# Kernel tuning notes

Measured on AMD Instinct MI355X. Metric: run time of the kernel, lower is better.

## Reference

```python
import jax, jax.numpy as jnp
import numpy as np

N = 50000      # nodes
E = 800000     # edges (avg degree 16)
F = 80         # hidden_channels (forced by Linear(80, 1))
L = 4          # num_layers
NG = 1024      # graphs in batch
NFEAT = 9      # OGB atom feature columns
VOCAB = 119    # max atom feature vocab
EPS_BN = 1e-5
EPS_STD = 1e-5


def setup_inputs() -> dict:
    key = jax.random.key(0)
    ks = jax.random.split(key, 20)
    s = 0.05
    x = jax.random.randint(ks[0], (N, NFEAT), 0, 2)
    edge_index = jax.random.randint(ks[1], (2, E), 0, N)
    batch = jnp.sort(jax.random.randint(ks[2], (N,), 0, NG))
    # avg_deg['log'] from the degree histogram == mean over nodes of log(deg+1)
    deg = jax.ops.segment_sum(jnp.ones((E,), jnp.float32), edge_index[1], num_segments=N)
    avg_deg_log = jnp.array([jnp.mean(jnp.log(deg + 1.0))], jnp.float32)
    atom_emb = jax.random.normal(ks[3], (NFEAT, VOCAB, F), jnp.float32) * s
    pre_W = jax.random.normal(ks[4], (L, 2 * F, F), jnp.float32) * s
    pre_b = jax.random.normal(ks[5], (L, F), jnp.float32) * s
    post_W = jax.random.normal(ks[6], (L, 13 * F, F), jnp.float32) * s
    post_b = jax.random.normal(ks[7], (L, F), jnp.float32) * s
    lin_W = jax.random.normal(ks[8], (L, F, F), jnp.float32) * s
    lin_b = jax.random.normal(ks[9], (L, F), jnp.float32) * s
    bn_gamma = 1.0 + jax.random.normal(ks[10], (L, F), jnp.float32) * 0.1
    bn_beta = jax.random.normal(ks[11], (L, F), jnp.float32) * 0.1
    bn_mean = jax.random.normal(ks[12], (L, F), jnp.float32) * 0.1
    bn_var = 0.5 + jax.random.uniform(ks[13], (L, F), jnp.float32)
    mlp_W = jax.random.normal(ks[14], (F, 1), jnp.float32) * s
    mlp_b = jax.random.normal(ks[15], (1,), jnp.float32) * s
    return {
        'x': x, 'edge_index': edge_index, 'batch': batch,
        'avg_deg_log': avg_deg_log, 'atom_emb': atom_emb,
        'pre_W': pre_W, 'pre_b': pre_b, 'post_W': post_W, 'post_b': post_b,
        'lin_W': lin_W, 'lin_b': lin_b,
        'bn_gamma': bn_gamma, 'bn_beta': bn_beta, 'bn_mean': bn_mean, 'bn_var': bn_var,
        'mlp_W': mlp_W, 'mlp_b': mlp_b,
    }


def _forward(x, edge_index, batch, avg_deg_log, atom_emb, pre_W, pre_b,
             post_W, post_b, lin_W, lin_b, bn_gamma, bn_beta, bn_mean, bn_var,
             mlp_W, mlp_b):
    # AtomEncoder: sum of per-column embeddings
    h = jnp.sum(atom_emb[jnp.arange(NFEAT)[None, :], x], axis=1)  # [N, F]
    src, dst = edge_index[0], edge_index[1]
    deg = jax.ops.segment_sum(jnp.ones((E,), h.dtype), dst, num_segments=N)
    has_edge = (deg > 0)[:, None]
    degc = jnp.maximum(deg, 1.0)[:, None]          # clamp(min=1)
    logd = jnp.log(degc + 1.0)                     # [N, 1]
    avg = avg_deg_log[0]
    for i in range(L):
        x_h = h
        # message: pre_nn(cat([x_i, x_j]))
        m = jnp.concatenate([h[dst], h[src]], axis=-1) @ pre_W[i] + pre_b[i]  # [E, F]
        s1 = jax.ops.segment_sum(m, dst, num_segments=N)
        s2 = jax.ops.segment_sum(m * m, dst, num_segments=N)
        mean = s1 / degc
        var = s2 / degc - mean * mean
        std = jnp.sqrt(jax.nn.relu(var) + EPS_STD)
        mn = jnp.where(has_edge, jax.ops.segment_min(m, dst, num_segments=N), 0.0)
        mx = jnp.where(has_edge, jax.ops.segment_max(m, dst, num_segments=N), 0.0)
        agg = jnp.concatenate([mean, mn, mx, std], axis=-1)  # [N, 4F]
        sc = logd / avg
        out = jnp.concatenate([agg, agg * sc, agg / sc], axis=-1)  # [N, 12F]
        out = jnp.concatenate([h, out], axis=-1) @ post_W[i] + post_b[i]  # [N, F]
        out = out @ lin_W[i] + lin_b[i]
        out = (out - bn_mean[i]) * (bn_gamma[i] / jnp.sqrt(bn_var[i] + EPS_BN)) + bn_beta[i]
        h = x_h + jax.nn.relu(out)  # dropout is identity in eval
    counts = jnp.maximum(jax.ops.segment_sum(jnp.ones((N,), h.dtype), batch, num_segments=NG), 1.0)
    g = jax.ops.segment_sum(h, batch, num_segments=NG) / counts[:, None]  # global_mean_pool
    return g @ mlp_W + mlp_b  # [NG, 1]


def reference(x, edge_index, batch, avg_deg_log, atom_emb, pre_W, pre_b,
              post_W, post_b, lin_W, lin_b, bn_gamma, bn_beta, bn_mean, bn_var,
              mlp_W, mlp_b):
    return _forward(x, edge_index, batch, avg_deg_log, atom_emb, pre_W, pre_b,
                    post_W, post_b, lin_W, lin_b, bn_gamma, bn_beta, bn_mean, bn_var,
                    mlp_W, mlp_b)
```

## Files before the change

### kernel.cpp

```cpp
#include <hip/hip_runtime.h>
#include <hip/hip_bf16.h>

#define NN 50000
#define NE 800000
#define FD 80
#define NGR 1024
#define NF 9

#define BSH 6
#define NBUCK ((NN + 63) >> 6)
#define CSH 12
#define NCH ((NE + 4095) >> 12)
#define BCAP 2048

using bf16 = __hip_bfloat16;
typedef __attribute__((ext_vector_type(8))) short bf16x8;
typedef __attribute__((ext_vector_type(4))) float f32x4;

static __device__ __forceinline__ float b2f(bf16 v){ return __bfloat162float(v); }
static __device__ __forceinline__ bf16 f2b(float v){ return __float2bfloat16(v); }
static __device__ __forceinline__ float rdw(const void* p, int i, int fl){
  return fl ? ((const float*)p)[i] : b2f(((const bf16*)p)[i]);
}
static __device__ __forceinline__ unsigned pk(float a, float b){
  bf16 x = f2b(a), y = f2b(b);
  return (unsigned)*(unsigned short*)&x | ((unsigned)*(unsigned short*)&y << 16);
}
static __device__ __forceinline__ bf16x8 ldsld8(const short* p){
  union { bf16x8 v; uint2 u[2]; } r;
  r.u[0] = *(const uint2*)(p);
  r.u[1] = *(const uint2*)(p + 4);
  return r.v;
}
static __device__ __forceinline__ void ldsst16(short* p, uint4 v){
  *(uint2*)(p)     = make_uint2(v.x, v.y);
  *(uint2*)(p + 4) = make_uint2(v.z, v.w);
}

__global__ void k_zero(int* __restrict__ p, int n){
  int t = blockIdx.x*256 + threadIdx.x;
  if (t < n) p[t] = 0;
}

__global__ void k_probe(const void* __restrict__ emb, int* __restrict__ flag){
  int t = blockIdx.x*256 + threadIdx.x;
  float v = b2f(((const bf16*)emb)[t]);
  if (!(fabsf(v) < 1e4f)) atomicOr(flag, 1);
}

__global__ __launch_bounds__(256) void k_prep_all(
    const void* __restrict__ preW, const void* __restrict__ preb,
    const void* __restrict__ postW, const void* __restrict__ postb,
    const void* __restrict__ linW, const void* __restrict__ linb,
    const void* __restrict__ bng, const void* __restrict__ bnb,
    const void* __restrict__ bnm, const void* __restrict__ bnv,
    const int* __restrict__ flag,
    bf16* __restrict__ pwb, bf16* __restrict__ Btl, bf16* __restrict__ Bt1,
    float* __restrict__ bias1, float* __restrict__ bias2)
{
  int fl = flag[0];
  int b = blockIdx.x;
  if (b < 1300){
    int t = b*256 + threadIdx.x;
    pwb[t] = f2b(rdw(postW, t, fl));
  } else if (b < 1420){
    int t = (b - 1300)*256 + threadIdx.x;
    int j = t % 96, c = (t/96) % 80, i = t/(96*80);
    float v = 0.f;
    if (j < 80){
      float gs = rdw(bng, i*80 + c, fl) * rsqrtf(rdw(bnv, i*80 + c, fl) + 1e-5f);
      v = rdw(linW, i*6400 + j*80 + c, fl) * gs;
    }
    Btl[t] = f2b(v);
  } else if (b < 1660){
    int t = (b - 1420)*256 + threadIdx.x;
    int k = t % 96, c = (t/96) % 160, i = t/(96*160);
    float v = 0.f;
    if (k < 80)
      v = (c < 80) ? rdw(preW, (i*160 + k)*80 + c, fl)
                   : rdw(preW, (i*160 + 80 + k)*80 + (c - 80), fl);
    int of = ((k >> 5)*160 + c)*32 + (k & 31);
    Bt1[i*15360 + of] = f2b(v);
    if (k == 0) bias1[i*160 + c] = (c < 80) ? rdw(preb, i*80 + c, fl) : 0.f;
  } else {
    int t = (b - 1660)*256 + threadIdx.x;
    if (t >= 4*80) return;
    int i = t / 80, f = t - i*80;
    float s = 0.f;
    for (int j = 0; j < 80; j++)
      s += rdw(postb, i*80 + j, fl) * rdw(linW, (i*80 + j)*80 + f, fl);
    s += rdw(linb, t, fl);
    float gs = rdw(bng, t, fl) * rsqrtf(rdw(bnv, t, fl) + 1e-5f);
    bias2[t] = (s - rdw(bnm, t, fl)) * gs + rdw(bnb, t, fl);
  }
}

__global__ void k_prep_Bt2(const float* __restrict__ Wf, bf16* __restrict__ Bt2){
  int t = blockIdx.x*256 + threadIdx.x;
  if (t >= 4*240*416) return;
  int k = t % 416;
  int c = (t/416) % 240;
  int i = t/(416*240);
  float v = 0.f;
  if (k < 400){
    int blk = c/80, f = c - blk*80;
    if (blk == 0) v = Wf[(i*1040 + k)*80 + f];
    else if (k >= 80){
      int row = (blk == 1 ? 400 : 720) + (k - 80);
      v = Wf[(i*1040 + row)*80 + f];
    }
  }
  int of = (k >> 5)*7680 + c*32 + (k & 31);
  Bt2[i*99840 + of] = f2b(v);
}

__global__ void k_atom(const int* __restrict__ x, const void* __restrict__ emb,
                       const int* __restrict__ flag, float* __restrict__ h){
  int fl = flag[0];
  int gid = blockIdx.x*256 + threadIdx.x;
  if (gid >= NN*10) return;
  int n = gid / 10, fb = gid - n*10;
  int f0 = fb*8;
  int xr[NF];
  #pragma unroll
  for (int c = 0; c < NF; c++) xr[c] = x[n*NF + c];
  float s[8] = {0.f,0.f,0.f,0.f,0.f,0.f,0.f,0.f};
  if (fl){
    #pragma unroll
    for (int c = 0; c < NF; c++){
      const float* ep = (const float*)emb + (c*119 + xr[c])*80 + f0;
      float4 a = *(const float4*)ep, b = *(const float4*)(ep + 4);
      s[0]+=a.x; s[1]+=a.y; s[2]+=a.z; s[3]+=a.w;
      s[4]+=b.x; s[5]+=b.y; s[6]+=b.z; s[7]+=b.w;
    }
  } else {
    #pragma unroll
    for (int c = 0; c < NF; c++){
      const bf16* ep = (const bf16*)emb + (c*119 + xr[c])*80 + f0;
      uint4 u = *(const uint4*)ep;
      s[0]+=__uint_as_float(u.x<<16); s[1]+=__uint_as_float(u.x&0xffff0000u);
      s[2]+=__uint_as_float(u.y<<16); s[3]+=__uint_as_float(u.y&0xffff0000u);
      s[4]+=__uint_as_float(u.z<<16); s[5]+=__uint_as_float(u.z&0xffff0000u);
      s[6]+=__uint_as_float(u.w<<16); s[7]+=__uint_as_float(u.w&0xffff0000u);
    }
  }
  float* hp = h + n*80 + f0;
  *(float4*)hp       = make_float4(s[0],s[1],s[2],s[3]);
  *(float4*)(hp + 4) = make_float4(s[4],s[5],s[6],s[7]);
}


__global__ __launch_bounds__(256) void k_hist(const int* __restrict__ ei,
                                              int* __restrict__ chunkcnt){
  __shared__ int hist[NBUCK];
  int c = blockIdx.x, t = threadIdx.x;
  for (int i = t; i < NBUCK; i += 256) hist[i] = 0;
  __syncthreads();
  #pragma unroll
  for (int j = 0; j < 16; j++){
    int e = (c << CSH) + j*256 + t;
    if (e < NE) atomicAdd(&hist[ei[NE + e] >> BSH], 1);
  }
  __syncthreads();
  for (int i = t; i < NBUCK; i += 256) chunkcnt[c*NBUCK + i] = hist[i];
}

__global__ __launch_bounds__(256) void k_cscan(int* __restrict__ chunkcnt,
                                               int* __restrict__ btotal){
  __shared__ int buf[256];
  int b = blockIdx.x, t = threadIdx.x;
  int v[4]; int s = 0;
  #pragma unroll
  for (int j = 0; j < 4; j++){
    int c = t*4 + j;
    v[j] = (c < NCH) ? chunkcnt[c*NBUCK + b] : 0;
    s += v[j];
  }
  buf[t] = s;
  __syncthreads();
  for (int off = 1; off < 256; off <<= 1){
    int xv = (t >= off) ? buf[t - off] : 0;
    __syncthreads();
    buf[t] += xv;
    __syncthreads();
  }
  int excl = buf[t] - s;
  #pragma unroll
  for (int j = 0; j < 4; j++){
    int c = t*4 + j;
    if (c < NCH){ chunkcnt[c*NBUCK + b] = excl; excl += v[j]; }
  }
  if (t == 255) btotal[b] = buf[255];
}

__global__ __launch_bounds__(256) void k_bscan(const int* __restrict__ btotal,
                                               int* __restrict__ bbase){
  __shared__ int buf[256];
  int t = threadIdx.x;
  int v[4]; int s = 0;
  #pragma unroll
  for (int j = 0; j < 4; j++){
    int c = t*4 + j;
    v[j] = (c < NBUCK) ? btotal[c] : 0;
    s += v[j];
  }
  buf[t] = s;
  __syncthreads();
  for (int off = 1; off < 256; off <<= 1){
    int xv = (t >= off) ? buf[t - off] : 0;
    __syncthreads();
    buf[t] += xv;
    __syncthreads();
  }
  int excl = buf[t] - s;
  #pragma unroll
  for (int j = 0; j < 4; j++){
    int c = t*4 + j;
    if (c < NBUCK){ bbase[c] = excl; excl += v[j]; }
  }
  if (t == 255) bbase[NBUCK] = buf[255];
}

__global__ __launch_bounds__(256) void k_place(const int* __restrict__ ei,
                        const int* __restrict__ chunkcnt, const int* __restrict__ bbase,
                        int* __restrict__ staging){
  __shared__ int basep[NBUCK];
  __shared__ int cur[NBUCK];
  int c = blockIdx.x, t = threadIdx.x;
  for (int i = t; i < NBUCK; i += 256){
    basep[i] = chunkcnt[c*NBUCK + i] + bbase[i];
    cur[i] = 0;
  }
  __syncthreads();
  #pragma unroll
  for (int j = 0; j < 16; j++){
    int e = (c << CSH) + j*256 + t;
    if (e < NE){
      int d = ei[NE + e], s = ei[e];
      int b = d >> BSH;
      int r = atomicAdd(&cur[b], 1);
      staging[basep[b] + r] = (s << BSH) | (d & 63);
    }
  }
}

__global__ __launch_bounds__(256) void k_csr(const int* __restrict__ staging,
                        const int* __restrict__ bbase, const void* __restrict__ avgp,
                        const int* __restrict__ flag, int* __restrict__ rowptr,
                        float* __restrict__ scf, float* __restrict__ invf,
                        int* __restrict__ colidx){
  __shared__ int lcnt[64], lrp[64], lcur[64];
  __shared__ int colbuf[BCAP];
  int b = blockIdx.x, t = threadIdx.x;
  int base = bbase[b];
  int cnt  = bbase[b+1] - base;
  if (t < 64){ lcnt[t] = 0; lcur[t] = 0; }
  __syncthreads();
  for (int i = t; i < cnt; i += 256)
    atomicAdd(&lcnt[staging[base + i] & 63], 1);
  __syncthreads();
  if (t < 64) lrp[t] = lcnt[t];
  __syncthreads();
  for (int off = 1; off < 64; off <<= 1){
    int xv = (t < 64 && t >= off) ? lrp[t - off] : 0;
    __syncthreads();
    if (t < 64) lrp[t] += xv;
    __syncthreads();
  }
  int n0 = b << BSH;
  if (t < 64){
    int ex = lrp[t] - lcnt[t];
    lrp[t] = ex;
    int n = n0 + t;
    if (n < NN){
      rowptr[n] = base + ex;
      float degc = (float)(lcnt[t] > 0 ? lcnt[t] : 1);
      float logd = logf(degc + 1.f);
      float avg = rdw(avgp, 0, flag[0]);
      scf[n] = logd / avg;
      invf[n] = avg / logd;
    }
  }
  if (b == 0 && t == 0) rowptr[NN] = NE;
  __syncthreads();
  if (cnt <= BCAP){
    for (int i = t; i < cnt; i += 256){
      int v = staging[base + i];
      int l = v & 63;
      int pos = lrp[l] + atomicAdd(&lcur[l], 1);
      colbuf[pos] = v >> BSH;
    }
    __syncthreads();
    for (int i = t; i < cnt; i += 256)
      colidx[base + i] = colbuf[i];
  } else {
    for (int i = t; i < cnt; i += 256){
      int v = staging[base + i];
      int l = v & 63;
      int pos = lrp[l] + atomicAdd(&lcur[l], 1);
      colidx[base + pos] = v >> BSH;
    }
  }
}

template<int AF32, int OUTMODE, int K_, int AST>
__global__ __launch_bounds__(256) void k_mgemm(
    const void* __restrict__ A1p, int s1, int KA,
    const bf16* __restrict__ A2, int s2, int KB,
    const bf16* __restrict__ Btp, int Bts, int Ncols,
    const float* __restrict__ bias,
    void* __restrict__ Cbase, void* __restrict__ Cp2, int Cstride, int M,
    int lA1b, int lBtb, int lCb)
{
  const void* A1 = (const char*)A1p + (size_t)blockIdx.z*lA1b;
  const bf16* Bt = (const bf16*)((const char*)Btp + (size_t)blockIdx.z*lBtb);
  void* Cp = (char*)Cbase + (size_t)blockIdx.z*lCb;

  constexpr int NKT = K_ / 32;
  __shared__ short As[64*AST];
  __shared__ short Bs[256*44];

  const int tid = threadIdx.x;
  const int row0 = blockIdx.x * 64;
  const int wave = tid >> 6, lane = tid & 63;
  const int wc = wave * 64;
  const int m16 = lane & 15, q = lane >> 4;

  const int ra = tid >> 2, ka = (tid & 3) * 8;
  const int cb = tid >> 2, kb = (tid & 3) * 8;

  f32x4 acc[4][4] = {};
  uint4 pb[4];

#define LOADB(k0_) { int kgb = (k0_) + kb;                                     \
    _Pragma("unroll")                                                          \
    for (int j = 0; j < 4; j++){                                               \
      int col = cb + j*64;                                                     \
      pb[j].x = pb[j].y = pb[j].z = pb[j].w = 0u;                              \
      if (col < Ncols) pb[j] = *(const uint4*)(Bt + col*Bts + kgb);            \
    } }

  LOADB(0);

  {
    const int grow = row0 + ra;
    uint4 tA[NKT];
    #pragma unroll
    for (int c = 0; c < NKT; c++){
      int kg = c*32 + ka;
      uint4 pa; pa.x = pa.y = pa.z = pa.w = 0u;
      if (grow < M){
        if (kg < KA){
          if (AF32){
            const float* ap = (const float*)A1 + grow*s1 + kg;
            float4 f0 = *(const float4*)ap;
            float4 f1 = *(const float4*)(ap + 4);
            pa.x = pk(f0.x, f0.y); pa.y = pk(f0.z, f0.w);
            pa.z = pk(f1.x, f1.y); pa.w = pk(f1.z, f1.w);
          } else {
            pa = *(const uint4*)((const bf16*)A1 + grow*s1 + kg);
          }
        } else if (kg - KA < KB){
          pa = *(const uint4*)(A2 + grow*s2 + (kg - KA));
        }
      }
      tA[c] = pa;
    }
    #pragma unroll
    for (int c = 0; c < NKT; c++)
      ldsst16(&As[ra*AST + c*32 + ka], tA[c]);
  }
  __syncthreads();

  #pragma unroll
  for (int ks = 0; ks < NKT; ks++){
    #pragma unroll
    for (int j = 0; j < 4; j++)
      ldsst16(&Bs[(cb + j*64)*44 + kb], pb[j]);
    __syncthreads();

    if (ks + 1 < NKT) LOADB((ks + 1)*32);

    bf16x8 af[4], bfv[4];
    #pragma unroll
    for (int rt = 0; rt < 4; rt++)
      af[rt] = ldsld8(&As[(rt*16 + m16)*AST + ks*32 + q*8]);
    #pragma unroll
    for (int ct = 0; ct < 4; ct++)
      bfv[ct] = ldsld8(&Bs[(wc + ct*16 + m16)*44 + q*8]);
    #pragma unroll
    for (int rt = 0; rt < 4; rt++)
      #pragma unroll
      for (int ct = 0; ct < 4; ct++)
        acc[rt][ct] = __builtin_amdgcn_mfma_f32_16x16x32_bf16(af[rt], bfv[ct], acc[rt][ct], 0, 0, 0);
    __syncthreads();
  }
#undef LOADB

  #pragma unroll
  for (int rt = 0; rt < 4; rt++){
    #pragma unroll
    for (int rr = 0; rr < 4; rr++){
      int row = row0 + rt*16 + q*4 + rr;
      if (row >= M) continue;
      #pragma unroll
      for (int ct = 0; ct < 4; ct++){
        int col = wc + ct*16 + m16;
        if (col >= Ncols) continue;
        float v = acc[rt][ct][rr] + (bias ? bias[col] : 0.f);
        if (OUTMODE == 1) ((float*)Cp)[row*Cstride + col] = v;
        else {
          if (col < 80) ((bf16*)Cp )[row*80 + col]      = f2b(v);
          else          ((bf16*)Cp2)[row*80 + col - 80] = f2b(v);
        }
      }
    }
  }
}

__global__ __launch_bounds__(256) void k_g1(
    const float* __restrict__ h, const bf16* __restrict__ Bt1t,
    const float* __restrict__ bias1v,
    bf16* __restrict__ Ua, bf16* __restrict__ Ub)
{
  __shared__ short hA[32*100];
  const int tid = threadIdx.x;
  const int row0 = blockIdx.x * 32;
  const int wave = tid >> 6, lane = tid & 63;
  const int wc = wave * 64;
  const int m16 = lane & 15, q = lane >> 4;
  const int ra = tid >> 3, ka0 = (tid & 7) * 8;

  {
    int grow = row0 + ra;
    #pragma unroll
    for (int c = 0; c < 2; c++){
      int kg = ka0 + c*64;
      if (kg < 96){
        uint4 pa; pa.x = pa.y = pa.z = pa.w = 0u;
        if (kg < 80 && grow < NN){
          const float* ap = h + grow*80 + kg;
          float4 f0 = *(const float4*)ap, f1 = *(const float4*)(ap + 4);
          pa.x = pk(f0.x, f0.y); pa.y = pk(f0.z, f0.w);
          pa.z = pk(f1.x, f1.y); pa.w = pk(f1.z, f1.w);
        }
        ldsst16(&hA[ra*100 + kg], pa);
      }
    }
  }
  __syncthreads();

  const bf16* bp1[4];
  #pragma unroll
  for (int ct = 0; ct < 4; ct++){
    int col = wc + ct*16 + m16;
    if (col >= 160) col = 0;
    bp1[ct] = Bt1t + col*32 + q*8;
  }
  f32x4 acc[2][4] = {};
  #pragma unroll
  for (int ks = 0; ks < 3; ks++){
    bf16x8 bfv[4], af[2];
    #pragma unroll
    for (int ct = 0; ct < 4; ct++)
      bfv[ct] = *(const bf16x8*)(bp1[ct] + ks*5120);
    #pragma unroll
    for (int rt = 0; rt < 2; rt++)
      af[rt] = ldsld8(&hA[(rt*16 + m16)*100 + ks*32 + q*8]);
    #pragma unroll
    for (int rt = 0; rt < 2; rt++)
      #pragma unroll
      for (int ct = 0; ct < 4; ct++)
        acc[rt][ct] = __builtin_amdgcn_mfma_f32_16x16x32_bf16(af[rt], bfv[ct], acc[rt][ct], 0, 0, 0);
  }
  #pragma unroll
  for (int rt = 0; rt < 2; rt++){
    #pragma unroll
    for (int rr = 0; rr < 4; rr++){
      int row = row0 + rt*16 + q*4 + rr;
      if (row >= NN) continue;
      #pragma unroll
      for (int ct = 0; ct < 4; ct++){
        int col = wc + ct*16 + m16;
        if (col >= 160) continue;
        float v = acc[rt][ct][rr] + bias1v[col];
        if (col < 80) Ua[row*80 + col]      = f2b(v);
        else          Ub[row*80 + col - 80] = f2b(v);
      }
    }
  }
}

__global__ __launch_bounds__(256) void k_g2(
    const float* __restrict__ h, const bf16* __restrict__ agg,
    const bf16* __restrict__ Bt, const float* __restrict__ bias2v,
    const float* __restrict__ scf, const float* __restrict__ invf,
    float* __restrict__ hp,
    const bf16* __restrict__ Bt1n, const float* __restrict__ bias1n,
    bf16* __restrict__ Ua, bf16* __restrict__ Ub)
{
  constexpr int AST = 420, NKT = 13;
  __shared__ short As[32*AST];
  bf16* eL = (bf16*)As;
  bf16* hA = (bf16*)(As + 8192);

  const int tid = threadIdx.x;
  const int row0 = blockIdx.x * 32;
  const int wave = tid >> 6, lane = tid & 63;
  const int wc = wave * 64;
  const int m16 = lane & 15, q = lane >> 4;
  const int ra = tid >> 3;
  const int ka0 = (tid & 7) * 8;

  {
    const int grow = row0 + ra;
    uint4 tA[7];
    #pragma unroll
    for (int c = 0; c < 7; c++){
      int kg = ka0 + c*64;
      uint4 pa; pa.x = pa.y = pa.z = pa.w = 0u;
      if (kg < 416 && grow < NN){
        if (kg < 80){
          const float* ap = h + grow*80 + kg;
          float4 f0 = *(const float4*)ap;
          float4 f1 = *(const float4*)(ap + 4);
          pa.x = pk(f0.x, f0.y); pa.y = pk(f0.z, f0.w);
          pa.z = pk(f1.x, f1.y); pa.w = pk(f1.z, f1.w);
        } else if (kg < 400){
          pa = *(const uint4*)(agg + grow*320 + (kg - 80));
        }
      }
      tA[c] = pa;
    }
    #pragma unroll
    for (int c = 0; c < 7; c++){
      int kg = ka0 + c*64;
      if (kg < 416) ldsst16(&As[ra*AST + kg], tA[c]);
    }
  }

  const bf16* bp[4];
  #pragma unroll
  for (int ct = 0; ct < 4; ct++){
    int col = wc + ct*16 + m16;
    if (col >= 240) col = 0;
    bp[ct] = Bt + col*32 + q*8;
  }
  __syncthreads();

  f32x4 acc[2][4] = {};

  #pragma unroll
  for (int ks = 0; ks < NKT; ks++){
    bf16x8 bfv[4], af[2];
    #pragma unroll
    for (int ct = 0; ct < 4; ct++)
      bfv[ct] = *(const bf16x8*)(bp[ct] + ks*7680);
    #pragma unroll
    for (int rt = 0; rt < 2; rt++)
      af[rt] = ldsld8(&As[(rt*16 + m16)*AST + ks*32 + q*8]);
    #pragma unroll
    for (int rt = 0; rt < 2; rt++)
      #pragma unroll
      for (int ct = 0; ct < 4; ct++)
        acc[rt][ct] = __builtin_amdgcn_mfma_f32_16x16x32_bf16(af[rt], bfv[ct], acc[rt][ct], 0, 0, 0);
  }
  __syncthreads();

  #pragma unroll
  for (int rt = 0; rt < 2; rt++){
    #pragma unroll
    for (int ct = 0; ct < 4; ct++){
      int col = wc + ct*16 + m16;
      if (col >= 240) continue;
      #pragma unroll
      for (int rr = 0; rr < 4; rr++){
        int r = rt*16 + q*4 + rr;
        eL[r*248 + col] = f2b(acc[rt][ct][rr]);
      }
    }
  }
  __syncthreads();

  #pragma unroll
  for (int i = 0; i < 10; i++){
    int idx = tid + i*256;
    int r = idx / 80, c = idx - r*80;
    int row = row0 + r;
    if (row < NN){
      float P = b2f(eL[r*248 + c]);
      float Q = b2f(eL[r*248 + 80 + c]);
      float R = b2f(eL[r*248 + 160 + c]);
      float o = P + scf[row]*Q + invf[row]*R + bias2v[c];
      float hn = hp[row*80 + c] + fmaxf(o, 0.f);
      hp[row*80 + c] = hn;
      if (Bt1n) hA[r*100 + c] = f2b(hn);
    } else if (Bt1n && idx < 32*80){
      hA[r*100 + c] = f2b(0.f);
    }
  }
  if (Bt1n && tid < 128){
    int r = tid >> 2, off = 80 + (tid & 3)*4;
    *(uint2*)&hA[r*100 + off] = make_uint2(0u, 0u);
  }
  __syncthreads();

  if (Bt1n){
    const bf16* bp1[4];
    #pragma unroll
    for (int ct = 0; ct < 4; ct++){
      int col = wc + ct*16 + m16;
      if (col >= 160) col = 0;
      bp1[ct] = Bt1n + col*32 + q*8;
    }
    f32x4 acc2[2][4] = {};
    #pragma unroll
    for (int ks = 0; ks < 3; ks++){
      bf16x8 bfv[4], af[2];
      #pragma unroll
      for (int ct = 0; ct < 4; ct++)
        bfv[ct] = *(const bf16x8*)(bp1[ct] + ks*5120);
      #pragma unroll
      for (int rt = 0; rt < 2; rt++)
        af[rt] = ldsld8((const short*)hA + (rt*16 + m16)*100 + ks*32 + q*8);
      #pragma unroll
      for (int rt = 0; rt < 2; rt++)
        #pragma unroll
        for (int ct = 0; ct < 4; ct++)
          acc2[rt][ct] = __builtin_amdgcn_mfma_f32_16x16x32_bf16(af[rt], bfv[ct], acc2[rt][ct], 0, 0, 0);
    }
    #pragma unroll
    for (int rt = 0; rt < 2; rt++){
      #pragma unroll
      for (int rr = 0; rr < 4; rr++){
        int row = row0 + rt*16 + q*4 + rr;
        if (row >= NN) continue;
        #pragma unroll
        for (int ct = 0; ct < 4; ct++){
          int col = wc + ct*16 + m16;
          if (col >= 160) continue;
          float v = acc2[rt][ct][rr] + bias1n[col];
          if (col < 80) Ua[row*80 + col]      = f2b(v);
          else          Ub[row*80 + col - 80] = f2b(v);
        }
      }
    }
  }
}

__global__ __launch_bounds__(256) void k_agg(const bf16* __restrict__ Ua,
                      const bf16* __restrict__ Ub,
                      const int* __restrict__ rowptr,
                      const int* __restrict__ colidx, bf16* __restrict__ agg)
{
  int lane = threadIdx.x & 63;
  int slot = lane / 20;
  int n = blockIdx.x*12 + (threadIdx.x >> 6)*3 + slot;
  if (slot >= 3 || n >= NN) return;
  int fo = (lane - slot*20) * 4;
  int rs = rowptr[n], re = rowptr[n+1];
  int deg = re - rs;

  float a[4];
  {
    uint2 ua = *(const uint2*)(Ua + n*80 + fo);
    a[0] = __uint_as_float(ua.x << 16);
    a[1] = __uint_as_float(ua.x & 0xffff0000u);
    a[2] = __uint_as_float(ua.y << 16);
    a[3] = __uint_as_float(ua.y & 0xffff0000u);
  }
  float sb[4] = {0.f,0.f,0.f,0.f}, sq[4] = {0.f,0.f,0.f,0.f};
  float mn[4] = {1e30f,1e30f,1e30f,1e30f}, mx[4] = {-1e30f,-1e30f,-1e30f,-1e30f};

#define ACC2(w, o) { \
    float b0 = __uint_as_float((w) << 16); \
    float b1 = __uint_as_float((w) & 0xffff0000u); \
    sb[o] += b0; sq[o] += b0*b0; mn[o] = fminf(mn[o],b0); mx[o] = fmaxf(mx[o],b0); \
    sb[o+1] += b1; sq[o+1] += b1*b1; mn[o+1] = fminf(mn[o+1],b1); mx[o+1] = fmaxf(mx[o+1],b1); }

  for (int e = rs; e < re; e += 16){
    int cnt = re - e; if (cnt > 16) cnt = 16;
    int s[16];
    #pragma unroll
    for (int j = 0; j < 16; j++) s[j] = (j < cnt) ? colidx[e + j] : s[0];
    uint2 u[16];
    #pragma unroll
    for (int j = 0; j < 16; j++) u[j] = *(const uint2*)(Ub + s[j]*80 + fo);
    #pragma unroll
    for (int j = 0; j < 16; j++){
      if (j < cnt){ ACC2(u[j].x, 0); ACC2(u[j].y, 2); }
    }
  }
#undef ACC2

  float degc = (float)(deg > 0 ? deg : 1);
  float inv = 1.f/degc;
  float dm = (float)deg;
  float mean0, mean1, v0, v1, sd0, sd1, lo0, lo1, hi0, hi1;

  mean0 = (dm*a[0] + sb[0])*inv; mean1 = (dm*a[1] + sb[1])*inv;
  v0 = (dm*a[0]*a[0] + 2.f*a[0]*sb[0] + sq[0])*inv - mean0*mean0;
  v1 = (dm*a[1]*a[1] + 2.f*a[1]*sb[1] + sq[1])*inv - mean1*mean1;
  sd0 = sqrtf(fmaxf(v0,0.f)+1e-5f); sd1 = sqrtf(fmaxf(v1,0.f)+1e-5f);
  lo0 = deg>0 ? a[0]+mn[0] : 0.f; lo1 = deg>0 ? a[1]+mn[1] : 0.f;
  hi0 = deg>0 ? a[0]+mx[0] : 0.f; hi1 = deg>0 ? a[1]+mx[1] : 0.f;
  unsigned o0 = pk(mean0, mean1);
  unsigned l0 = pk(lo0, lo1), h0 = pk(hi0, hi1), t0 = pk(sd0, sd1);

  mean0 = (dm*a[2] + sb[2])*inv; mean1 = (dm*a[3] + sb[3])*inv;
  v0 = (dm*a[2]*a[2] + 2.f*a[2]*sb[2] + sq[2])*inv - mean0*mean0;
  v1 = (dm*a[3]*a[3] + 2.f*a[3]*sb[3] + sq[3])*inv - mean1*mean1;
  sd0 = sqrtf(fmaxf(v0,0.f)+1e-5f); sd1 = sqrtf(fmaxf(v1,0.f)+1e-5f);
  lo0 = deg>0 ? a[2]+mn[2] : 0.f; lo1 = deg>0 ? a[3]+mn[3] : 0.f;
  hi0 = deg>0 ? a[2]+mx[2] : 0.f; hi1 = deg>0 ? a[3]+mx[3] : 0.f;
  unsigned o1 = pk(mean0, mean1);
  unsigned l1 = pk(lo0, lo1), h1 = pk(hi0, hi1), t1 = pk(sd0, sd1);

  bf16* ag = agg + n*320 + fo;
  *(uint2*)(ag)       = make_uint2(o0, o1);
  *(uint2*)(ag + 80)  = make_uint2(l0, l1);
  *(uint2*)(ag + 160) = make_uint2(h0, h1);
  *(uint2*)(ag + 240) = make_uint2(t0, t1);
}

__global__ __launch_bounds__(128) void k_poolmlp(const float* __restrict__ h,
                        const int* __restrict__ batch,
                        const void* __restrict__ mlpW, const void* __restrict__ mlpb,
                        const int* __restrict__ flag, void* __restrict__ outp){
  __shared__ float sred[128];
  __shared__ int sb[2];
  int g = blockIdx.x;
  int t = threadIdx.x;
  if (t < 2){
    int target = g + t;
    int lo = 0, hi = NN;
    while (lo < hi){ int mid = (lo + hi) >> 1; if (batch[mid] < target) lo = mid + 1; else hi = mid; }
    sb[t] = lo;
  }
  __syncthreads();
  int lo = sb[0], hi = sb[1];
  float s = 0.f;
  if (t < 80)
    for (int n = lo; n < hi; n++) s += h[n*80 + t];
  int fl = flag[0];
  float wv = (t < 80) ? rdw(mlpW, t, fl) : 0.f;
  sred[t] = s * wv;
  __syncthreads();
  for (int off = 64; off > 0; off >>= 1){
    if (t < off) sred[t] += sred[t + off];
    __syncthreads();
  }
  if (t == 0){
    float cnt = (float)(hi - lo); if (cnt < 1.f) cnt = 1.f;
    float r = sred[0]/cnt + rdw(mlpb, 0, fl);
    if (fl) ((float*)outp)[g] = r;
    else    ((bf16*)outp)[g] = f2b(r);
  }
}

extern "C" void kernel_launch(void* const* d_in, const int* in_sizes, int n_in,
                              void* d_out, int out_size, void* d_ws, size_t ws_size,
                              hipStream_t stream)
{
  const int*  x     = (const int*) d_in[0];
  const int*  ei    = (const int*) d_in[1];
  const int*  batch = (const int*) d_in[2];
  const void* avgp  = d_in[3];
  const void* aemb  = d_in[4];
  const void* preW  = d_in[5];
  const void* preb  = d_in[6];
  const void* postW = d_in[7];
  const void* postb = d_in[8];
  const void* linW  = d_in[9];
  const void* linb  = d_in[10];
  const void* bng   = d_in[11];
  const void* bnb   = d_in[12];
  const void* bnm   = d_in[13];
  const void* bnv   = d_in[14];
  const void* mlpW  = d_in[15];
  const void* mlpb  = d_in[16];

  char* w = (char*)d_ws;
  int*   flag   = (int*)  (w + 400000);
  int*   rowptr = (int*)  (w + 401280);
  int*   colidx = (int*)  (w + 601344);
  float* scf    = (float*)(w + 3801344);
  float* invf   = (float*)(w + 4001344);
  float* bias1  = (float*)(w + 4201344);
  float* bias2  = (float*)(w + 4203904);
  bf16*  Btl    = (bf16*) (w + 4205184);
  bf16*  Bt1    = (bf16*) (w + 4266624);
  bf16*  Bt2    = (bf16*) (w + 4389504);
  float* h      = (float*)(w + 5188224);
  bf16*  Ua     = (bf16*) (w + 21188224);
  bf16*  Ub     = (bf16*) (w + 29188224);
  bf16*  agg    = (bf16*) (w + 45188224);
  bf16*  pwb    = (bf16*) (w + 45188224);
  float* Wf     = (float*)(w + 45853824);
  int* staging  = (int*)  (w + 47185024);
  int* chunkcnt = (int*)  (w + 50385024);
  int* btotal   = (int*)  (w + 52831120);
  int* bbase    = (int*)  (w + 52834248);

  k_zero <<<1, 256, 0, stream>>>(flag, 64);
  k_probe<<<16, 256, 0, stream>>>(aemb, flag);

  k_hist <<<NCH, 256, 0, stream>>>(ei, chunkcnt);
  k_cscan<<<NBUCK, 256, 0, stream>>>(chunkcnt, btotal);
  k_bscan<<<1, 256, 0, stream>>>(btotal, bbase);
  k_place<<<NCH, 256, 0, stream>>>(ei, chunkcnt, bbase, staging);

  k_prep_all<<<1662, 256, 0, stream>>>(preW, preb, postW, postb, linW, linb,
                                       bng, bnb, bnm, bnv, flag,
                                       pwb, Btl, Bt1, bias1, bias2);

  k_mgemm<0,1,96,100><<<dim3(17,1,4), 256, 0, stream>>>(
      pwb, 80, 80, nullptr, 0, 0,
      Btl, 96, 80, nullptr, Wf, nullptr, 80, 1040,
      166400, 15360, 332800);
  k_prep_Bt2<<<(4*240*416 + 255)/256, 256, 0, stream>>>(Wf, Bt2);

  k_atom <<<(NN*10 + 255)/256, 256, 0, stream>>>(x, aemb, flag, h);

  k_csr<<<NBUCK, 256, 0, stream>>>(staging, bbase, avgp, flag, rowptr, scf, invf, colidx);

  const int gx2 = (NN + 31)/32;
  k_g1<<<dim3(gx2,1,1), 256, 0, stream>>>(h, Bt1, bias1, Ua, Ub);
  for (int i = 0; i < 4; i++){
    k_agg<<<(NN + 11)/12, 256, 0, stream>>>(Ua, Ub, rowptr, colidx, agg);
    const bf16* nBt1   = (i < 3) ? (Bt1 + (i+1)*15360) : nullptr;
    const float* nb1   = (i < 3) ? (bias1 + (i+1)*160) : bias1;
    k_g2<<<dim3(gx2,1,1), 256, 0, stream>>>(
        h, agg, Bt2 + i*99840, bias2 + i*80, scf, invf, h,
        nBt1, nb1, Ua, Ub);
  }

  k_poolmlp<<<NGR, 128, 0, stream>>>(h, batch, mlpW, mlpb, flag, d_out);
}
```

Measured before the change: 523.6 us.

## Fuse neighbor aggregation into post-GEMM kernel with ping-pong U buffers

Removes the separate k_agg kernel and computes mean/min/max/std aggregation directly into LDS inside k_g2, so the bf16 agg tensor is no longer written to and read back from global memory. Because k_g2 now gathers Ub from neighbors while also writing next-layer Ua/Ub, the buffers are double-buffered (A/B swapped per layer) to avoid read/write races across blocks. In exchange, the gather phase runs only 240 of 256 threads across three rounds inside a GEMM kernel, which may lower gather parallelism and occupancy compared with the dedicated kernel.

New measurement: 514.8 us. Within noise of the previous version (-1.7%).

```diff
diff --git a/kernel.cpp b/kernel.cpp
--- a/kernel.cpp
+++ b/kernel.cpp
@@ -492,15 +492,18 @@
 }
 
 __global__ __launch_bounds__(256) void k_g2(
-    const float* __restrict__ h, const bf16* __restrict__ agg,
+    const float* __restrict__ h,
+    const bf16* __restrict__ Uar, const bf16* __restrict__ Ubr,
+    const int* __restrict__ rowptr, const int* __restrict__ colidx,
     const bf16* __restrict__ Bt, const float* __restrict__ bias2v,
     const float* __restrict__ scf, const float* __restrict__ invf,
     float* __restrict__ hp,
     const bf16* __restrict__ Bt1n, const float* __restrict__ bias1n,
-    bf16* __restrict__ Ua, bf16* __restrict__ Ub)
+    bf16* __restrict__ Uaw, bf16* __restrict__ Ubw)
 {
   constexpr int AST = 420, NKT = 13;
   __shared__ short As[32*AST];
+  __shared__ int nrp[33];
   bf16* eL = (bf16*)As;
   bf16* hA = (bf16*)(As + 8192);
 
@@ -512,31 +515,101 @@
   const int ra = tid >> 3;
   const int ka0 = (tid & 7) * 8;
 
+  if (tid < 33){
+    int n = row0 + tid;
+    nrp[tid] = rowptr[n < NN ? n : NN];
+  }
+
   {
     const int grow = row0 + ra;
-    uint4 tA[7];
     #pragma unroll
     for (int c = 0; c < 7; c++){
       int kg = ka0 + c*64;
-      uint4 pa; pa.x = pa.y = pa.z = pa.w = 0u;
-      if (kg < 416 && grow < NN){
-        if (kg < 80){
+      if (kg < 80){
+        uint4 pa; pa.x = pa.y = pa.z = pa.w = 0u;
+        if (grow < NN){
           const float* ap = h + grow*80 + kg;
           float4 f0 = *(const float4*)ap;
           float4 f1 = *(const float4*)(ap + 4);
           pa.x = pk(f0.x, f0.y); pa.y = pk(f0.z, f0.w);
           pa.z = pk(f1.x, f1.y); pa.w = pk(f1.z, f1.w);
-        } else if (kg < 400){
-          pa = *(const uint4*)(agg + grow*320 + (kg - 80));
+        }
+        ldsst16(&As[ra*AST + kg], pa);
+      } else if (kg >= 400 && kg < 416){
+        uint4 z; z.x = z.y = z.z = z.w = 0u;
+        ldsst16(&As[ra*AST + kg], z);
+      }
+    }
+  }
+  __syncthreads();
+
+  {
+    int s20 = tid / 20;
+    int fo = (tid - s20*20) * 4;
+#define ACC2(w, o) { \
+    float b0 = __uint_as_float((w) << 16); \
+    float b1 = __uint_as_float((w) & 0xffff0000u); \
+    sb[o] += b0; sq[o] += b0*b0; mn[o] = fminf(mn[o],b0); mx[o] = fmaxf(mx[o],b0); \
+    sb[o+1] += b1; sq[o+1] += b1*b1; mn[o+1] = fminf(mn[o+1],b1); mx[o+1] = fmaxf(mx[o+1],b1); }
+    #pragma unroll 1
+    for (int rnd = 0; rnd < 3; rnd++){
+      int slot = rnd*12 + s20;
+      if (s20 < 12 && slot < 32){
+        int n = row0 + slot;
+        short* st = &As[slot*AST + 80 + fo];
+        if (n < NN){
+          int rs = nrp[slot], re = nrp[slot+1];
+          int deg = re - rs;
+          float a[4];
+          {
+            uint2 ua = *(const uint2*)(Uar + n*80 + fo);
+            a[0] = __uint_as_float(ua.x << 16);
+            a[1] = __uint_as_float(ua.x & 0xffff0000u);
+            a[2] = __uint_as_float(ua.y << 16);
+            a[3] = __uint_as_float(ua.y & 0xffff0000u);
+          }
+          float sb[4] = {0.f,0.f,0.f,0.f}, sq[4] = {0.f,0.f,0.f,0.f};
+          float mn[4] = {1e30f,1e30f,1e30f,1e30f}, mx[4] = {-1e30f,-1e30f,-1e30f,-1e30f};
+          for (int e = rs; e < re; e += 16){
+            int cnt = re - e; if (cnt > 16) cnt = 16;
+            int sx[16];
+            #pragma unroll
+            for (int j = 0; j < 16; j++) sx[j] = (j < cnt) ? colidx[e + j] : sx[0];
+            uint2 u[16];
+            #pragma unroll
+            for (int j = 0; j < 16; j++) u[j] = *(const uint2*)(Ubr + sx[j]*80 + fo);
+            #pragma unroll
+            for (int j = 0; j < 16; j++){
+              if (j < cnt){ ACC2(u[j].x, 0); ACC2(u[j].y, 2); }
+            }
+          }
+          float degc = (float)(deg > 0 ? deg : 1);
+          float inv = 1.f/degc;
+          float dm = (float)deg;
+          float mean[4], lo[4], hi[4], sd[4];
+          #pragma unroll
+          for (int i = 0; i < 4; i++){
+            float av = a[i];
+            mean[i] = (dm*av + sb[i])*inv;
+            float vv = (dm*av*av + 2.f*av*sb[i] + sq[i])*inv - mean[i]*mean[i];
+            sd[i] = sqrtf(fmaxf(vv, 0.f) + 1e-5f);
+            lo[i] = deg > 0 ? av + mn[i] : 0.f;
+            hi[i] = deg > 0 ? av + mx[i] : 0.f;
+          }
+          *(uint2*)(st)       = make_uint2(pk(mean[0],mean[1]), pk(mean[2],mean[3]));
+          *(uint2*)(st +  80) = make_uint2(pk(lo[0],lo[1]),     pk(lo[2],lo[3]));
+          *(uint2*)(st + 160) = make_uint2(pk(hi[0],hi[1]),     pk(hi[2],hi[3]));
+          *(uint2*)(st + 240) = make_uint2(pk(sd[0],sd[1]),     pk(sd[2],sd[3]));
+        } else {
+          uint2 z = make_uint2(0u, 0u);
+          *(uint2*)(st)       = z;
+          *(uint2*)(st +  80) = z;
+          *(uint2*)(st + 160) = z;
+          *(uint2*)(st + 240) = z;
         }
       }
-      tA[c] = pa;
-    }
-    #pragma unroll
-    for (int c = 0; c < 7; c++){
-      int kg = ka0 + c*64;
-      if (kg < 416) ldsst16(&As[ra*AST + kg], tA[c]);
-    }
+    }
+#undef ACC2
   }
 
   const bf16* bp[4];
@@ -640,87 +713,12 @@
           int col = wc + ct*16 + m16;
           if (col >= 160) continue;
           float v = acc2[rt][ct][rr] + bias1n[col];
-          if (col < 80) Ua[row*80 + col]      = f2b(v);
-          else          Ub[row*80 + col - 80] = f2b(v);
+          if (col < 80) Uaw[row*80 + col]      = f2b(v);
+          else          Ubw[row*80 + col - 80] = f2b(v);
         }
       }
     }
   }
-}
-
-__global__ __launch_bounds__(256) void k_agg(const bf16* __restrict__ Ua,
-                      const bf16* __restrict__ Ub,
-                      const int* __restrict__ rowptr,
-                      const int* __restrict__ colidx, bf16* __restrict__ agg)
-{
-  int lane = threadIdx.x & 63;
-  int slot = lane / 20;
-  int n = blockIdx.x*12 + (threadIdx.x >> 6)*3 + slot;
-  if (slot >= 3 || n >= NN) return;
-  int fo = (lane - slot*20) * 4;
-  int rs = rowptr[n], re = rowptr[n+1];
-  int deg = re - rs;
-
-  float a[4];
-  {
-    uint2 ua = *(const uint2*)(Ua + n*80 + fo);
-    a[0] = __uint_as_float(ua.x << 16);
-    a[1] = __uint_as_float(ua.x & 0xffff0000u);
-    a[2] = __uint_as_float(ua.y << 16);
-    a[3] = __uint_as_float(ua.y & 0xffff0000u);
-  }
-  float sb[4] = {0.f,0.f,0.f,0.f}, sq[4] = {0.f,0.f,0.f,0.f};
-  float mn[4] = {1e30f,1e30f,1e30f,1e30f}, mx[4] = {-1e30f,-1e30f,-1e30f,-1e30f};
-
-#define ACC2(w, o) { \
-    float b0 = __uint_as_float((w) << 16); \
-    float b1 = __uint_as_float((w) & 0xffff0000u); \
-    sb[o] += b0; sq[o] += b0*b0; mn[o] = fminf(mn[o],b0); mx[o] = fmaxf(mx[o],b0); \
-    sb[o+1] += b1; sq[o+1] += b1*b1; mn[o+1] = fminf(mn[o+1],b1); mx[o+1] = fmaxf(mx[o+1],b1); }
-
-  for (int e = rs; e < re; e += 16){
-    int cnt = re - e; if (cnt > 16) cnt = 16;
-    int s[16];
-    #pragma unroll
-    for (int j = 0; j < 16; j++) s[j] = (j < cnt) ? colidx[e + j] : s[0];
-    uint2 u[16];
-    #pragma unroll
-    for (int j = 0; j < 16; j++) u[j] = *(const uint2*)(Ub + s[j]*80 + fo);
-    #pragma unroll
-    for (int j = 0; j < 16; j++){
-      if (j < cnt){ ACC2(u[j].x, 0); ACC2(u[j].y, 2); }
-    }
-  }
-#undef ACC2
-
-  float degc = (float)(deg > 0 ? deg : 1);
-  float inv = 1.f/degc;
-  float dm = (float)deg;
-  float mean0, mean1, v0, v1, sd0, sd1, lo0, lo1, hi0, hi1;
-
-  mean0 = (dm*a[0] + sb[0])*inv; mean1 = (dm*a[1] + sb[1])*inv;
-  v0 = (dm*a[0]*a[0] + 2.f*a[0]*sb[0] + sq[0])*inv - mean0*mean0;
-  v1 = (dm*a[1]*a[1] + 2.f*a[1]*sb[1] + sq[1])*inv - mean1*mean1;
-  sd0 = sqrtf(fmaxf(v0,0.f)+1e-5f); sd1 = sqrtf(fmaxf(v1,0.f)+1e-5f);
-  lo0 = deg>0 ? a[0]+mn[0] : 0.f; lo1 = deg>0 ? a[1]+mn[1] : 0.f;
-  hi0 = deg>0 ? a[0]+mx[0] : 0.f; hi1 = deg>0 ? a[1]+mx[1] : 0.f;
-  unsigned o0 = pk(mean0, mean1);
-  unsigned l0 = pk(lo0, lo1), h0 = pk(hi0, hi1), t0 = pk(sd0, sd1);
-
-  mean0 = (dm*a[2] + sb[2])*inv; mean1 = (dm*a[3] + sb[3])*inv;
-  v0 = (dm*a[2]*a[2] + 2.f*a[2]*sb[2] + sq[2])*inv - mean0*mean0;
-  v1 = (dm*a[3]*a[3] + 2.f*a[3]*sb[3] + sq[3])*inv - mean1*mean1;
-  sd0 = sqrtf(fmaxf(v0,0.f)+1e-5f); sd1 = sqrtf(fmaxf(v1,0.f)+1e-5f);
-  lo0 = deg>0 ? a[2]+mn[2] : 0.f; lo1 = deg>0 ? a[3]+mn[3] : 0.f;
-  hi0 = deg>0 ? a[2]+mx[2] : 0.f; hi1 = deg>0 ? a[3]+mx[3] : 0.f;
-  unsigned o1 = pk(mean0, mean1);
-  unsigned l1 = pk(lo0, lo1), h1 = pk(hi0, hi1), t1 = pk(sd0, sd1);
-
-  bf16* ag = agg + n*320 + fo;
-  *(uint2*)(ag)       = make_uint2(o0, o1);
-  *(uint2*)(ag + 80)  = make_uint2(l0, l1);
-  *(uint2*)(ag + 160) = make_uint2(h0, h1);
-  *(uint2*)(ag + 240) = make_uint2(t0, t1);
 }
 
 __global__ __launch_bounds__(128) void k_poolmlp(const float* __restrict__ h,
@@ -792,15 +790,16 @@
   bf16*  Bt1    = (bf16*) (w + 4266624);
   bf16*  Bt2    = (bf16*) (w + 4389504);
   float* h      = (float*)(w + 5188224);
-  bf16*  Ua     = (bf16*) (w + 21188224);
-  bf16*  Ub     = (bf16*) (w + 29188224);
-  bf16*  agg    = (bf16*) (w + 45188224);
-  bf16*  pwb    = (bf16*) (w + 45188224);
-  float* Wf     = (float*)(w + 45853824);
-  int* staging  = (int*)  (w + 47185024);
-  int* chunkcnt = (int*)  (w + 50385024);
-  int* btotal   = (int*)  (w + 52831120);
-  int* bbase    = (int*)  (w + 52834248);
+  bf16*  UaA    = (bf16*) (w + 21188224);
+  bf16*  UbA    = (bf16*) (w + 29188224);
+  bf16*  UaB    = (bf16*) (w + 45188224);
+  bf16*  UbB    = (bf16*) (w + 53188224);
+  bf16*  pwb    = (bf16*) (w + 61188224);
+  float* Wf     = (float*)(w + 61853824);
+  int* staging  = (int*)  (w + 63185024);
+  int* chunkcnt = (int*)  (w + 66385024);
+  int* btotal   = (int*)  (w + 66998112);
+  int* bbase    = (int*)  (w + 67001240);
 
   k_zero <<<1, 256, 0, stream>>>(flag, 64);
   k_probe<<<16, 256, 0, stream>>>(aemb, flag);
@@ -825,14 +824,18 @@
   k_csr<<<NBUCK, 256, 0, stream>>>(staging, bbase, avgp, flag, rowptr, scf, invf, colidx);
 
   const int gx2 = (NN + 31)/32;
-  k_g1<<<dim3(gx2,1,1), 256, 0, stream>>>(h, Bt1, bias1, Ua, Ub);
+  k_g1<<<dim3(gx2,1,1), 256, 0, stream>>>(h, Bt1, bias1, UaA, UbA);
   for (int i = 0; i < 4; i++){
-    k_agg<<<(NN + 11)/12, 256, 0, stream>>>(Ua, Ub, rowptr, colidx, agg);
-    const bf16* nBt1   = (i < 3) ? (Bt1 + (i+1)*15360) : nullptr;
-    const float* nb1   = (i < 3) ? (bias1 + (i+1)*160) : bias1;
+    const bf16* Uar = (i & 1) ? UaB : UaA;
+    const bf16* Ubr = (i & 1) ? UbB : UbA;
+    bf16* Uaw = (i & 1) ? UaA : UaB;
+    bf16* Ubw = (i & 1) ? UbA : UbB;
+    const bf16* nBt1 = (i < 3) ? (Bt1 + (i+1)*15360) : nullptr;
+    const float* nb1 = (i < 3) ? (bias1 + (i+1)*160) : bias1;
     k_g2<<<dim3(gx2,1,1), 256, 0, stream>>>(
-        h, agg, Bt2 + i*99840, bias2 + i*80, scf, invf, h,
-        nBt1, nb1, Ua, Ub);
+        h, Uar, Ubr, rowptr, colidx,
+        Bt2 + i*99840, bias2 + i*80, scf, invf, h,
+        nBt1, nb1, Uaw, Ubw);
   }
 
   k_poolmlp<<<NGR, 128, 0, stream>>>(h, batch, mlpW, mlpb, flag, d_out);
```
